# Optimization experiments

Hardware: AMD Instinct MI355X
Metric: run time of the kernel (lower is better)

Reference implementation:

```python
import jax, jax.numpy as jnp
import numpy as np

FREQ = 10000.0

def _abs_pos(T, d, freq):
    # AP[t, 2i] = sin(t / freq**(2i/d)), AP[t, 2i+1] = cos(...), i in [0, T//2)
    pos = jnp.arange(T, dtype=jnp.float32)[:, None]          # [T,1]
    i = jnp.arange(T // 2, dtype=jnp.float32)[None, :]       # [1,T/2]
    angle = pos / (freq ** (2.0 * i / d))                    # [T,T/2]
    return jnp.stack([jnp.sin(angle), jnp.cos(angle)], axis=-1).reshape(T, T)

def setup_inputs() -> dict:
    key = jax.random.key(0)
    k0, k1, k2, k3, k4 = jax.random.split(key, 5)
    T, d, H, dh = 4096, 1024, 8, 128
    s = 1.0 / np.sqrt(d).astype(np.float32)
    return {
        "x": jax.random.normal(k0, (T, d), jnp.float32),
        "Wq": jax.random.normal(k1, (H, dh, d), jnp.float32) * s,
        "Wk": jax.random.normal(k2, (H, dh, d), jnp.float32) * s,
        "Wv": jax.random.normal(k3, (H, dh, d), jnp.float32) * s,
        "Wout": jax.random.normal(k4, (d, H * dh), jnp.float32) * s,
    }

def reference(x, Wq, Wk, Wv, Wout):
    # x: [T,d]; Wq/Wk/Wv: [H,dh,d] (torch Linear weight layout, bias=False); Wout: [d, H*dh]
    T, d = x.shape
    Q = jnp.einsum('td,hed->hte', x, Wq)                     # [H,T,dh]
    K = jnp.einsum('td,hed->hte', x, Wk)
    V = jnp.einsum('td,hed->hte', x, Wv)
    energies = jnp.einsum('hte,hse->hts', Q, K)              # [H,T,T] (no 1/sqrt(dh) scaling, as in source)
    energies = energies + _abs_pos(T, d, FREQ)[None]         # absolute sinusoidal bias added to scores
    att = jax.nn.softmax(energies, axis=-1)                  # [H,T,T]
    # dropout(p=0.5) is identity in eval mode; reference runs in eval mode
    y = jnp.einsum('hts,hse->hte', att, V)                   # [H,T,dh]
    y = jnp.transpose(y, (1, 0, 2)).reshape(T, -1)           # concat heads along feature dim -> [T, H*dh]
    y = y @ Wout.T                                           # [T,d]
    return y, att[-1]                                        # source returns last head's att_weights
```

## Files before the change

### kernel.cpp

```cpp
#include <hip/hip_runtime.h>
#include <math.h>

#define Tn 4096
#define Dm 1024
#define Hn 8
#define DH 128

typedef __bf16 bf16x8 __attribute__((ext_vector_type(8)));
typedef float f32x4 __attribute__((ext_vector_type(4)));

#define LOG2E 1.4426950408889634f
#define WEXP 0.025952563241307518f
#define WDECAY 0.31622776601683794f
#define PIO2 1.5707963267948966f

#define MFMA(a, b, c) __builtin_amdgcn_mfma_f32_16x16x32_bf16((a), (b), (c), 0, 0, 0)

#define GLOAD_LDS(g, l) __builtin_amdgcn_global_load_lds( \
    (__attribute__((address_space(1))) void*)(void*)(g),  \
    (__attribute__((address_space(3))) void*)(l), 16, 0, 0)

__global__ __launch_bounds__(256)
void split_kernel(const float* __restrict__ in, __bf16* __restrict__ hi,
                  __bf16* __restrict__ lo, int n4) {
    int idx = blockIdx.x * 256 + threadIdx.x;
    if (idx >= n4) return;
    float4 v = ((const float4*)in)[idx];
    __attribute__((aligned(8))) __bf16 h[4], l[4];
    h[0] = (__bf16)v.x; h[1] = (__bf16)v.y; h[2] = (__bf16)v.z; h[3] = (__bf16)v.w;
    l[0] = (__bf16)(v.x - (float)h[0]);
    l[1] = (__bf16)(v.y - (float)h[1]);
    l[2] = (__bf16)(v.z - (float)h[2]);
    l[3] = (__bf16)(v.w - (float)h[3]);
    *(float2*)&hi[(size_t)idx * 4] = *(float2*)h;
    *(float2*)&lo[(size_t)idx * 4] = *(float2*)l;
}

__global__ __launch_bounds__(256)
void vtrans_kernel(const __bf16* __restrict__ V, __bf16* __restrict__ Vt) {
    __shared__ __bf16 tile[64][80];
    int h = blockIdx.z, t0 = blockIdx.x * 64, e0 = blockIdx.y * 64;
    const __bf16* Vh = V + (size_t)h * Tn * DH;
    __bf16* Vth = Vt + (size_t)h * DH * Tn;
#pragma unroll
    for (int p = 0; p < 2; ++p) {
        int r = (threadIdx.x >> 3) + p * 32;
        int c = (threadIdx.x & 7) * 8;
        *(float4*)&tile[r][c] = *(const float4*)&Vh[(size_t)(t0 + r) * DH + e0 + c];
    }
    __syncthreads();
#pragma unroll
    for (int p = 0; p < 2; ++p) {
        int r = (threadIdx.x >> 3) + p * 32;
        int c = (threadIdx.x & 7) * 8;
        __attribute__((aligned(16))) __bf16 tmp[8];
#pragma unroll
        for (int j = 0; j < 8; ++j) tmp[j] = tile[c + j][r];
        *(float4*)&Vth[(size_t)(e0 + r) * Tn + t0 + c] = *(float4*)tmp;
    }
}

__device__ __forceinline__
void gemm_body(__bf16 (*smem)[128 * 32],
               const __bf16* __restrict__ Ahi, const __bf16* __restrict__ Alo,
               const __bf16* __restrict__ Bhi, const __bf16* __restrict__ Blo,
               int ldA, int ldB, int K, int m0, int n0, f32x4 acc[4][4]) {
    int tid = threadIdx.x;
    int lane = tid & 63, wid = tid >> 6;
    int wm = (wid >> 1) * 64, wn = (wid & 1) * 64;
    int lm = lane & 15, q = lane >> 4;
    int lr = lane >> 2;
    int lc = (lane & 3) * 8;
    const bool split = (Alo != nullptr);
    for (int k0 = 0; k0 < K; k0 += 32) {
        __syncthreads();
#pragma unroll
        for (int p = 0; p < 128; p += 64) {
            int rb = p + wid * 16;
            int r = rb + lr;
            GLOAD_LDS(&Ahi[(size_t)(m0 + r) * ldA + k0 + lc], &smem[0][rb * 32]);
            GLOAD_LDS(&Bhi[(size_t)(n0 + r) * ldB + k0 + lc], &smem[2][rb * 32]);
            if (split) {
                GLOAD_LDS(&Alo[(size_t)(m0 + r) * ldA + k0 + lc], &smem[1][rb * 32]);
                GLOAD_LDS(&Blo[(size_t)(n0 + r) * ldB + k0 + lc], &smem[3][rb * 32]);
            }
        }
        __syncthreads();
        bf16x8 ah[4], bh[4], al[4], bl[4];
#pragma unroll
        for (int mt = 0; mt < 4; ++mt) {
            ah[mt] = *(const bf16x8*)&smem[0][(wm + mt * 16 + lm) * 32 + q * 8];
            if (split)
                al[mt] = *(const bf16x8*)&smem[1][(wm + mt * 16 + lm) * 32 + q * 8];
        }
#pragma unroll
        for (int nt = 0; nt < 4; ++nt) {
            bh[nt] = *(const bf16x8*)&smem[2][(wn + nt * 16 + lm) * 32 + q * 8];
            if (split)
                bl[nt] = *(const bf16x8*)&smem[3][(wn + nt * 16 + lm) * 32 + q * 8];
        }
#pragma unroll
        for (int mt = 0; mt < 4; ++mt)
#pragma unroll
            for (int nt = 0; nt < 4; ++nt) {
                acc[mt][nt] = MFMA(ah[mt], bh[nt], acc[mt][nt]);
                if (split) {
                    acc[mt][nt] = MFMA(ah[mt], bl[nt], acc[mt][nt]);
                    acc[mt][nt] = MFMA(al[mt], bh[nt], acc[mt][nt]);
                }
            }
    }
}

__global__ __launch_bounds__(256)
void qkv_kernel(const __bf16* __restrict__ xhi, const __bf16* __restrict__ xlo,
                const __bf16* __restrict__ Wqh, const __bf16* __restrict__ Wql,
                const __bf16* __restrict__ Wkh, const __bf16* __restrict__ Wkl,
                const __bf16* __restrict__ Wvh, const __bf16* __restrict__ Wvl,
                __bf16* __restrict__ Qh, __bf16* __restrict__ Ql,
                __bf16* __restrict__ Kh, __bf16* __restrict__ Kl,
                __bf16* __restrict__ Vb) {
    __shared__ __align__(16) __bf16 smem[4][128 * 32];
    int z = blockIdx.z;
    const __bf16* Bh = (z == 0) ? Wqh : (z == 1) ? Wkh : Wvh;
    const __bf16* Bl = (z == 0) ? Wql : (z == 1) ? Wkl : Wvl;
    __bf16* Oh = (z == 0) ? Qh : (z == 1) ? Kh : Vb;
    __bf16* Ol = (z == 0) ? Ql : (z == 1) ? Kl : nullptr;
    int m0 = blockIdx.y * 128, n0 = blockIdx.x * 128;
    int tid = threadIdx.x, lane = tid & 63, wid = tid >> 6;
    int wm = (wid >> 1) * 64, wn = (wid & 1) * 64;
    int lm = lane & 15, q = lane >> 4;
    f32x4 acc[4][4];
#pragma unroll
    for (int i = 0; i < 4; ++i)
#pragma unroll
        for (int j = 0; j < 4; ++j) acc[i][j] = (f32x4){0.f, 0.f, 0.f, 0.f};
    gemm_body(smem, xhi, xlo, Bh, Bl, Dm, Dm, Dm, m0, n0, acc);
#pragma unroll
    for (int mt = 0; mt < 4; ++mt)
#pragma unroll
        for (int r = 0; r < 4; ++r) {
            int grow = m0 + wm + mt * 16 + q * 4 + r;
#pragma unroll
            for (int nt = 0; nt < 4; ++nt) {
                int gc = n0 + wn + nt * 16 + lm;
                int h = gc >> 7, e = gc & 127;
                size_t o = ((size_t)h * Tn + grow) * DH + e;
                float v = acc[mt][nt][r];
                __bf16 hv = (__bf16)v;
                Oh[o] = hv;
                if (Ol) Ol[o] = (__bf16)(v - (float)hv);
            }
        }
}

__global__ __launch_bounds__(256)
void gemm_out(const __bf16* __restrict__ Ahi, const __bf16* __restrict__ Alo,
              const __bf16* __restrict__ Bhi, const __bf16* __restrict__ Blo,
              float* __restrict__ C) {
    __shared__ __align__(16) __bf16 smem[4][128 * 32];
    int m0 = blockIdx.y * 128, n0 = blockIdx.x * 128;
    int tid = threadIdx.x, lane = tid & 63, wid = tid >> 6;
    int wm = (wid >> 1) * 64, wn = (wid & 1) * 64;
    int lm = lane & 15, q = lane >> 4;
    f32x4 acc[4][4];
#pragma unroll
    for (int i = 0; i < 4; ++i)
#pragma unroll
        for (int j = 0; j < 4; ++j) acc[i][j] = (f32x4){0.f, 0.f, 0.f, 0.f};
    gemm_body(smem, Ahi, Alo, Bhi, Blo, Dm, Dm, Dm, m0, n0, acc);
#pragma unroll
    for (int mt = 0; mt < 4; ++mt)
#pragma unroll
        for (int r = 0; r < 4; ++r) {
            int grow = m0 + wm + mt * 16 + q * 4 + r;
#pragma unroll
            for (int nt = 0; nt < 4; ++nt)
                C[(size_t)grow * Dm + n0 + wn + nt * 16 + lm] = acc[mt][nt][r];
        }
}

__global__ __launch_bounds__(256, 2)
void flash_kernel(const __bf16* __restrict__ Qhi, const __bf16* __restrict__ Qlo,
                  const __bf16* __restrict__ Khi, const __bf16* __restrict__ Klo,
                  const __bf16* __restrict__ Vt, float* __restrict__ Opart,
                  float* __restrict__ mPart, float* __restrict__ lPart) {
    __shared__ __bf16 Ks[2][2][128][40];
    __shared__ __bf16 Ps[64][132];
    int bid = blockIdx.x;
    int h = bid & 7;
    int g = (bid >> 3) & 1;
    int m0 = (bid >> 4) * 64;
    int it0 = g * 16;
    const size_t TD = (size_t)Tn * DH;
    const __bf16* Qh = Qhi + h * TD;
    const __bf16* Ql = Qlo + h * TD;
    const __bf16* Kh = Khi + h * TD;
    const __bf16* Kl = Klo + h * TD;
    const __bf16* Vh = Vt + h * TD;
    float* Og = Opart + (size_t)g * Tn * Dm;

    int tid = threadIdx.x;
    int lane = tid & 63, wid = tid >> 6;
    int lm = lane & 15, q = lane >> 4;
    int wr0 = wid * 16;

    bf16x8 qfh[4], qfl[4];
#pragma unroll
    for (int kc = 0; kc < 4; ++kc) {
        size_t o = (size_t)(m0 + wr0 + lm) * DH + kc * 32 + q * 8;
        qfh[kc] = *(const bf16x8*)&Qh[o];
        qfl[kc] = *(const bf16x8*)&Ql[o];
    }

    f32x4 accO[8];
#pragma unroll
    for (int nt = 0; nt < 8; ++nt) accO[nt] = (f32x4){0.f, 0.f, 0.f, 0.f};
    float mrow[4], lrow[4];
#pragma unroll
    for (int r = 0; r < 4; ++r) { mrow[r] = -3.0e38f; lrow[r] = 0.f; }

    int sr = tid >> 2;
    int scc = (tid & 3) * 8;
    bool iscos = (lm & 1);
    float wv[8];
#pragma unroll
    for (int nt = 0; nt < 8; ++nt)
        wv[nt] = exp2f(-(float)(((g << 11) + nt * 16 + lm) >> 1) * WEXP);
    float tf[4];
#pragma unroll
    for (int r = 0; r < 4; ++r) tf[r] = (float)(m0 + wr0 + q * 4 + r);

    size_t voff[8];
#pragma unroll
    for (int nt = 0; nt < 8; ++nt)
        voff[nt] = (size_t)(nt * 16 + lm) * Tn + q * 8;

    float4 kh0, kl0, kh1, kl1;
    {
        size_t go0 = (size_t)(it0 * 128 + sr) * DH + scc;
        size_t go1 = go0 + (size_t)64 * DH;
        kh0 = *(const float4*)&Kh[go0];
        kl0 = *(const float4*)&Kl[go0];
        kh1 = *(const float4*)&Kh[go1];
        kl1 = *(const float4*)&Kl[go1];
    }

    for (int it = it0; it < it0 + 16; ++it) {
        int s0 = it * 128;
        f32x4 accS[8];
#pragma unroll
        for (int nt = 0; nt < 8; ++nt) accS[nt] = (f32x4){0.f, 0.f, 0.f, 0.f};

#pragma unroll
        for (int kc = 0; kc < 4; ++kc) {
            int b = kc & 1;
            *(float4*)&Ks[b][0][sr][scc]      = kh0;
            *(float4*)&Ks[b][1][sr][scc]      = kl0;
            *(float4*)&Ks[b][0][sr + 64][scc] = kh1;
            *(float4*)&Ks[b][1][sr + 64][scc] = kl1;
            __syncthreads();
            {
                int itn = (kc < 3) ? it : ((it < it0 + 15) ? it + 1 : it);
                int kcn = (kc < 3) ? kc + 1 : 0;
                size_t go0 = (size_t)(itn * 128 + sr) * DH + kcn * 32 + scc;
                size_t go1 = go0 + (size_t)64 * DH;
                kh0 = *(const float4*)&Kh[go0];
                kl0 = *(const float4*)&Kl[go0];
                kh1 = *(const float4*)&Kh[go1];
                kl1 = *(const float4*)&Kl[go1];
            }
            __builtin_amdgcn_s_setprio(1);
#pragma unroll
            for (int nt = 0; nt < 8; ++nt) {
                bf16x8 bh = *(const bf16x8*)&Ks[b][0][nt * 16 + lm][q * 8];
                bf16x8 bl = *(const bf16x8*)&Ks[b][1][nt * 16 + lm][q * 8];
                accS[nt] = MFMA(qfh[kc], bh, accS[nt]);
                accS[nt] = MFMA(qfh[kc], bl, accS[nt]);
                accS[nt] = MFMA(qfl[kc], bh, accS[nt]);
            }
            __builtin_amdgcn_s_setprio(0);
        }

        bf16x8 vrel[8];
#pragma unroll
        for (int nt = 0; nt < 8; ++nt)
            vrel[nt] = *(const bf16x8*)&Vh[voff[nt] + s0];

        float rmax[4];
#pragma unroll
        for (int r = 0; r < 4; ++r) {
            float mx = -3.0e38f;
#pragma unroll
            for (int nt = 0; nt < 8; ++nt) {
                float ang = tf[r] * wv[nt];
                float b = __sinf(iscos ? ang + PIO2 : ang);
                float v = accS[nt][r] + b;
                accS[nt][r] = v;
                mx = fmaxf(mx, v);
            }
            rmax[r] = mx;
        }
#pragma unroll
        for (int off = 1; off < 16; off <<= 1)
#pragma unroll
            for (int r = 0; r < 4; ++r)
                rmax[r] = fmaxf(rmax[r], __shfl_xor(rmax[r], off));
        float alpha[4], rsum[4];
#pragma unroll
        for (int r = 0; r < 4; ++r) {
            float mn = fmaxf(mrow[r], rmax[r]);
            alpha[r] = exp2f((mrow[r] - mn) * LOG2E);
            mrow[r] = mn;
            rsum[r] = 0.f;
        }
#pragma unroll
        for (int nt = 0; nt < 8; ++nt)
#pragma unroll
            for (int r = 0; r < 4; ++r) {
                float p = exp2f((accS[nt][r] - mrow[r]) * LOG2E);
                accS[nt][r] = p;
                rsum[r] += p;
            }
#pragma unroll
        for (int off = 1; off < 16; off <<= 1)
#pragma unroll
            for (int r = 0; r < 4; ++r)
                rsum[r] += __shfl_xor(rsum[r], off);
#pragma unroll
        for (int r = 0; r < 4; ++r)
            lrow[r] = lrow[r] * alpha[r] + rsum[r];
#pragma unroll
        for (int nt = 0; nt < 8; ++nt)
#pragma unroll
            for (int r = 0; r < 4; ++r)
                accO[nt][r] *= alpha[r];

#pragma unroll
        for (int nt = 0; nt < 8; ++nt)
#pragma unroll
            for (int r = 0; r < 4; ++r)
                Ps[wr0 + q * 4 + r][nt * 16 + lm] = (__bf16)accS[nt][r];

#pragma unroll
        for (int kc = 0; kc < 4; ++kc) {
            bf16x8 pa = *(const bf16x8*)&Ps[wr0 + lm][kc * 32 + q * 8];
            bf16x8 vcur[8];
#pragma unroll
            for (int nt = 0; nt < 8; ++nt) vcur[nt] = vrel[nt];
            if (kc < 3) {
#pragma unroll
                for (int nt = 0; nt < 8; ++nt)
                    vrel[nt] = *(const bf16x8*)&Vh[voff[nt] + s0 + (kc + 1) * 32];
            }
            __builtin_amdgcn_s_setprio(1);
#pragma unroll
            for (int nt = 0; nt < 8; ++nt)
                accO[nt] = MFMA(pa, vcur[nt], accO[nt]);
            __builtin_amdgcn_s_setprio(0);
        }

#pragma unroll
        for (int nt = 0; nt < 8; ++nt) wv[nt] *= WDECAY;
    }

#pragma unroll
    for (int r = 0; r < 4; ++r) {
        int t = m0 + wr0 + q * 4 + r;
#pragma unroll
        for (int nt = 0; nt < 8; ++nt)
            Og[(size_t)t * Dm + h * DH + nt * 16 + lm] = accO[nt][r];
        if (lm == 0) {
            mPart[(size_t)(g * Hn + h) * Tn + t] = mrow[r];
            lPart[(size_t)(g * Hn + h) * Tn + t] = lrow[r];
        }
    }
}

__global__ __launch_bounds__(256)
void combine_kernel(const float* __restrict__ Opart,
                    const float* __restrict__ mPart, const float* __restrict__ lPart,
                    __bf16* __restrict__ yhi, __bf16* __restrict__ ylo,
                    float* __restrict__ mM, float* __restrict__ lL) {
    int idx = blockIdx.x * 256 + threadIdx.x;
    int t = idx >> 8;
    int c4 = idx & 255;
    int c = c4 * 4;
    int h = c >> 7;
    float m0 = mPart[(size_t)h * Tn + t];
    float m1 = mPart[(size_t)(Hn + h) * Tn + t];
    float l0 = lPart[(size_t)h * Tn + t];
    float l1 = lPart[(size_t)(Hn + h) * Tn + t];
    float m = fmaxf(m0, m1);
    float w0 = exp2f((m0 - m) * LOG2E);
    float w1 = exp2f((m1 - m) * LOG2E);
    float l = l0 * w0 + l1 * w1;
    float inv = 1.0f / l;
    w0 *= inv; w1 *= inv;
    float4 a = ((const float4*)Opart)[idx];
    float4 b = ((const float4*)(Opart + (size_t)Tn * Dm))[idx];
    float y[4] = {a.x * w0 + b.x * w1, a.y * w0 + b.y * w1,
                  a.z * w0 + b.z * w1, a.w * w0 + b.w * w1};
    __attribute__((aligned(8))) __bf16 hh[4], ll[4];
#pragma unroll
    for (int j = 0; j < 4; ++j) {
        hh[j] = (__bf16)y[j];
        ll[j] = (__bf16)(y[j] - (float)hh[j]);
    }
    *(float2*)&yhi[(size_t)idx * 4] = *(float2*)hh;
    *(float2*)&ylo[(size_t)idx * 4] = *(float2*)ll;
    if (h == 7 && (c & 127) == 0) { mM[t] = m; lL[t] = l; }
}

__global__ __launch_bounds__(256)
void att_kernel(const __bf16* __restrict__ Ahi, const __bf16* __restrict__ Alo,
                const __bf16* __restrict__ Bhi, const __bf16* __restrict__ Blo,
                const float* __restrict__ mM, const float* __restrict__ lL,
                float* __restrict__ att) {
    __shared__ __align__(16) char shraw[34816];
    __bf16 (*smem)[128 * 32] = reinterpret_cast<__bf16(*)[128 * 32]>(shraw);
    float (*Ls)[68] = reinterpret_cast<float(*)[68]>(shraw);

    int m0 = blockIdx.y * 128, n0 = blockIdx.x * 128;
    int tid = threadIdx.x, lane = tid & 63, wid = tid >> 6;
    int wm = (wid >> 1) * 64, wn = (wid & 1) * 64;
    int lm = lane & 15, q = lane >> 4;
    f32x4 acc[4][4];
#pragma unroll
    for (int i = 0; i < 4; ++i)
#pragma unroll
        for (int j = 0; j < 4; ++j) acc[i][j] = (f32x4){0.f, 0.f, 0.f, 0.f};
    gemm_body(smem, Ahi, Alo, Bhi, Blo, DH, DH, DH, m0, n0, acc);

    float wv[4];
#pragma unroll
    for (int nt = 0; nt < 4; ++nt) {
        int s = n0 + wn + nt * 16 + lm;
        wv[nt] = exp2f(-(float)(s >> 1) * WEXP);
    }
    int par = lm & 1;
#pragma unroll
    for (int mt = 0; mt < 4; ++mt)
#pragma unroll
        for (int r = 0; r < 4; ++r) {
            int t = m0 + wm + mt * 16 + q * 4 + r;
            float tf = (float)t;
            float mr = mM[t];
            float linv = 1.0f / lL[t];
#pragma unroll
            for (int nt = 0; nt < 4; ++nt) {
                float ang = tf * wv[nt];
                float bias = __sinf(par ? ang + PIO2 : ang);
                acc[mt][nt][r] = exp2f((acc[mt][nt][r] + bias - mr) * LOG2E) * linv;
            }
        }

#pragma unroll
    for (int p = 0; p < 2; ++p) {
        __syncthreads();
        if ((wid & 1) == p) {
#pragma unroll
            for (int mt = 0; mt < 4; ++mt)
#pragma unroll
                for (int r = 0; r < 4; ++r)
#pragma unroll
                    for (int nt = 0; nt < 4; ++nt)
                        Ls[wm + mt * 16 + q * 4 + r][nt * 16 + lm] = acc[mt][nt][r];
        }
        __syncthreads();
#pragma unroll
        for (int j = 0; j < 8; ++j) {
            int row = j * 16 + (tid >> 4);
            int col = (tid & 15) * 4;
            float4 v = *(float4*)&Ls[row][col];
            *(float4*)&att[(size_t)(m0 + row) * Tn + n0 + p * 64 + col] = v;
        }
    }
}

extern "C" void kernel_launch(void* const* d_in, const int* in_sizes, int n_in,
                              void* d_out, int out_size, void* d_ws, size_t ws_size,
                              hipStream_t stream) {
    (void)in_sizes; (void)n_in; (void)out_size; (void)ws_size;
    const float* x    = (const float*)d_in[0];
    const float* Wq   = (const float*)d_in[1];
    const float* Wk   = (const float*)d_in[2];
    const float* Wv   = (const float*)d_in[3];
    const float* Wout = (const float*)d_in[4];

    float* out_y   = (float*)d_out;
    float* out_att = out_y + (size_t)Tn * Dm;

    const size_t MB = 1ull << 20;
    char* W = (char*)d_ws;
    __bf16* xhi  = (__bf16*)(W + 0 * MB);
    __bf16* xlo  = (__bf16*)(W + 8 * MB);
    __bf16* Wqhi = (__bf16*)(W + 16 * MB);
    __bf16* Wqlo = (__bf16*)(W + 18 * MB);
    __bf16* Wkhi = (__bf16*)(W + 20 * MB);
    __bf16* Wklo = (__bf16*)(W + 22 * MB);
    __bf16* Wvhi = (__bf16*)(W + 24 * MB);
    __bf16* Wvlo = (__bf16*)(W + 26 * MB);
    __bf16* Wohi = (__bf16*)(W + 28 * MB);
    __bf16* Wolo = (__bf16*)(W + 30 * MB);
    __bf16* Qhi  = (__bf16*)(W + 32 * MB);
    __bf16* Qlo  = (__bf16*)(W + 40 * MB);
    __bf16* Khi  = (__bf16*)(W + 48 * MB);
    __bf16* Klo  = (__bf16*)(W + 56 * MB);
    __bf16* Vb   = (__bf16*)(W + 64 * MB);
    __bf16* Vt   = (__bf16*)(W + 72 * MB);
    float*  mM    = (float*)(W + 80 * MB);
    float*  lL    = (float*)(W + 81 * MB);
    float*  mPart = (float*)(W + 82 * MB);
    float*  lPart = (float*)(W + 83 * MB);
    float*  Opart = (float*)(W + 84 * MB);
    __bf16* yhhi  = (__bf16*)(W + 116 * MB);
    __bf16* yhlo  = (__bf16*)(W + 124 * MB);

    dim3 blk(256);

    split_kernel<<<dim3(Tn * Dm / 4 / 256), blk, 0, stream>>>(x, xhi, xlo, Tn * Dm / 4);
    split_kernel<<<dim3(Dm * Dm / 4 / 256), blk, 0, stream>>>(Wq, Wqhi, Wqlo, Dm * Dm / 4);
    split_kernel<<<dim3(Dm * Dm / 4 / 256), blk, 0, stream>>>(Wk, Wkhi, Wklo, Dm * Dm / 4);
    split_kernel<<<dim3(Dm * Dm / 4 / 256), blk, 0, stream>>>(Wv, Wvhi, Wvlo, Dm * Dm / 4);
    split_kernel<<<dim3(Dm * Dm / 4 / 256), blk, 0, stream>>>(Wout, Wohi, Wolo, Dm * Dm / 4);

    qkv_kernel<<<dim3(Dm / 128, Tn / 128, 3), blk, 0, stream>>>(
        xhi, xlo, Wqhi, Wqlo, Wkhi, Wklo, Wvhi, Wvlo,
        Qhi, Qlo, Khi, Klo, Vb);
    vtrans_kernel<<<dim3(Tn / 64, DH / 64, Hn), blk, 0, stream>>>(Vb, Vt);

    flash_kernel<<<dim3(1024), blk, 0, stream>>>(Qhi, Qlo, Khi, Klo, Vt,
                                                 Opart, mPart, lPart);

    combine_kernel<<<dim3(Tn * Dm / 4 / 256), blk, 0, stream>>>(
        Opart, mPart, lPart, yhhi, yhlo, mM, lL);

    const size_t TD = (size_t)Tn * DH;
    att_kernel<<<dim3(Tn / 128, Tn / 128), blk, 0, stream>>>(
        Qhi + 7 * TD, Qlo + 7 * TD, Khi + 7 * TD, Klo + 7 * TD, mM, lL, out_att);

    gemm_out<<<dim3(Dm / 128, Tn / 128), blk, 0, stream>>>(yhhi, yhlo, Wohi, Wolo, out_y);
}
```

Measured before the change: 610.0 us.

## Stage QKV epilogue through LDS for coalesced stores; prefetch K two chunks ahead

The QKV projection epilogue now writes the bf16 hi and lo tiles into shared memory first, then stores whole 128-byte rows to global memory with vector writes, replacing scattered 2-byte stores. In the flash kernel, K chunks are register-prefetched two stages ahead using two alternating register sets instead of one, which gives each global load more time to arrive before its LDS write. This costs extra barriers in the epilogue and more registers in the flash kernel, which runs at two blocks per SM.

```diff
diff --git a/kernel.cpp b/kernel.cpp
--- a/kernel.cpp
+++ b/kernel.cpp
@@ -136,22 +136,48 @@
 #pragma unroll
         for (int j = 0; j < 4; ++j) acc[i][j] = (f32x4){0.f, 0.f, 0.f, 0.f};
     gemm_body(smem, xhi, xlo, Bh, Bl, Dm, Dm, Dm, m0, n0, acc);
+
+    __bf16* St = (__bf16*)smem;
+    int h0 = n0 >> 7;
+    int row = tid >> 1, half = (tid & 1) * 64;
+
+    __syncthreads();
 #pragma unroll
     for (int mt = 0; mt < 4; ++mt)
 #pragma unroll
-        for (int r = 0; r < 4; ++r) {
-            int grow = m0 + wm + mt * 16 + q * 4 + r;
-#pragma unroll
-            for (int nt = 0; nt < 4; ++nt) {
-                int gc = n0 + wn + nt * 16 + lm;
-                int h = gc >> 7, e = gc & 127;
-                size_t o = ((size_t)h * Tn + grow) * DH + e;
-                float v = acc[mt][nt][r];
-                __bf16 hv = (__bf16)v;
-                Oh[o] = hv;
-                if (Ol) Ol[o] = (__bf16)(v - (float)hv);
-            }
-        }
+        for (int r = 0; r < 4; ++r)
+#pragma unroll
+            for (int nt = 0; nt < 4; ++nt)
+                St[(wm + mt * 16 + q * 4 + r) * 128 + wn + nt * 16 + lm] =
+                    (__bf16)acc[mt][nt][r];
+    __syncthreads();
+    {
+        __bf16* dst = Oh + ((size_t)h0 * Tn + m0 + row) * DH + half;
+        const __bf16* src = St + row * 128 + half;
+#pragma unroll
+        for (int j = 0; j < 8; ++j)
+            *(float4*)&dst[j * 8] = *(const float4*)&src[j * 8];
+    }
+    if (Ol) {
+        __syncthreads();
+#pragma unroll
+        for (int mt = 0; mt < 4; ++mt)
+#pragma unroll
+            for (int r = 0; r < 4; ++r)
+#pragma unroll
+                for (int nt = 0; nt < 4; ++nt) {
+                    float v = acc[mt][nt][r];
+                    __bf16 hv = (__bf16)v;
+                    St[(wm + mt * 16 + q * 4 + r) * 128 + wn + nt * 16 + lm] =
+                        (__bf16)(v - (float)hv);
+                }
+        __syncthreads();
+        __bf16* dst = Ol + ((size_t)h0 * Tn + m0 + row) * DH + half;
+        const __bf16* src = St + row * 128 + half;
+#pragma unroll
+        for (int j = 0; j < 8; ++j)
+            *(float4*)&dst[j * 8] = *(const float4*)&src[j * 8];
+    }
 }
 
 __global__ __launch_bounds__(256)
@@ -179,6 +205,33 @@
                 C[(size_t)grow * Dm + n0 + wn + nt * 16 + lm] = acc[mt][nt][r];
         }
 }
+
+#define QK_STEP(SET, BUF, QIDX, NIT, NKC)                                     \
+    {                                                                          \
+        *(float4*)&Ks[BUF][0][sr][scc]      = SET##h0;                         \
+        *(float4*)&Ks[BUF][1][sr][scc]      = SET##l0;                         \
+        *(float4*)&Ks[BUF][0][sr + 64][scc] = SET##h1;                         \
+        *(float4*)&Ks[BUF][1][sr + 64][scc] = SET##l1;                         \
+        __syncthreads();                                                       \
+        {                                                                      \
+            size_t go0 = (size_t)((NIT) * 128 + sr) * DH + (NKC) * 32 + scc;   \
+            size_t go1 = go0 + (size_t)64 * DH;                                \
+            SET##h0 = *(const float4*)&Kh[go0];                                \
+            SET##l0 = *(const float4*)&Kl[go0];                                \
+            SET##h1 = *(const float4*)&Kh[go1];                                \
+            SET##l1 = *(const float4*)&Kl[go1];                                \
+        }                                                                      \
+        __builtin_amdgcn_s_setprio(1);                                         \
+        _Pragma("unroll")                                                      \
+        for (int nt = 0; nt < 8; ++nt) {                                       \
+            bf16x8 kbh = *(const bf16x8*)&Ks[BUF][0][nt * 16 + lm][q * 8];     \
+            bf16x8 kbl = *(const bf16x8*)&Ks[BUF][1][nt * 16 + lm][q * 8];     \
+            accS[nt] = MFMA(qfh[QIDX], kbh, accS[nt]);                         \
+            accS[nt] = MFMA(qfh[QIDX], kbl, accS[nt]);                         \
+            accS[nt] = MFMA(qfl[QIDX], kbh, accS[nt]);                         \
+        }                                                                      \
+        __builtin_amdgcn_s_setprio(0);                                         \
+    }
 
 __global__ __launch_bounds__(256, 2)
 void flash_kernel(const __bf16* __restrict__ Qhi, const __bf16* __restrict__ Qlo,
@@ -236,51 +289,28 @@
     for (int nt = 0; nt < 8; ++nt)
         voff[nt] = (size_t)(nt * 16 + lm) * Tn + q * 8;
 
-    float4 kh0, kl0, kh1, kl1;
+    float4 kah0, kal0, kah1, kal1, kbh0, kbl0, kbh1, kbl1;
     {
-        size_t go0 = (size_t)(it0 * 128 + sr) * DH + scc;
-        size_t go1 = go0 + (size_t)64 * DH;
-        kh0 = *(const float4*)&Kh[go0];
-        kl0 = *(const float4*)&Kl[go0];
-        kh1 = *(const float4*)&Kh[go1];
-        kl1 = *(const float4*)&Kl[go1];
+        size_t g0 = (size_t)(it0 * 128 + sr) * DH + scc;
+        size_t g1 = g0 + (size_t)64 * DH;
+        kah0 = *(const float4*)&Kh[g0]; kal0 = *(const float4*)&Kl[g0];
+        kah1 = *(const float4*)&Kh[g1]; kal1 = *(const float4*)&Kl[g1];
+        size_t h0_ = g0 + 32, h1_ = g1 + 32;
+        kbh0 = *(const float4*)&Kh[h0_]; kbl0 = *(const float4*)&Kl[h0_];
+        kbh1 = *(const float4*)&Kh[h1_]; kbl1 = *(const float4*)&Kl[h1_];
     }
 
     for (int it = it0; it < it0 + 16; ++it) {
         int s0 = it * 128;
+        int itn = (it < it0 + 15) ? it + 1 : it;
         f32x4 accS[8];
 #pragma unroll
         for (int nt = 0; nt < 8; ++nt) accS[nt] = (f32x4){0.f, 0.f, 0.f, 0.f};
 
-#pragma unroll
-        for (int kc = 0; kc < 4; ++kc) {
-            int b = kc & 1;
-            *(float4*)&Ks[b][0][sr][scc]      = kh0;
-            *(float4*)&Ks[b][1][sr][scc]      = kl0;
-            *(float4*)&Ks[b][0][sr + 64][scc] = kh1;
-            *(float4*)&Ks[b][1][sr + 64][scc] = kl1;
-            __syncthreads();
-            {
-                int itn = (kc < 3) ? it : ((it < it0 + 15) ? it + 1 : it);
-                int kcn = (kc < 3) ? kc + 1 : 0;
-                size_t go0 = (size_t)(itn * 128 + sr) * DH + kcn * 32 + scc;
-                size_t go1 = go0 + (size_t)64 * DH;
-                kh0 = *(const float4*)&Kh[go0];
-                kl0 = *(const float4*)&Kl[go0];
-                kh1 = *(const float4*)&Kh[go1];
-                kl1 = *(const float4*)&Kl[go1];
-            }
-            __builtin_amdgcn_s_setprio(1);
-#pragma unroll
-            for (int nt = 0; nt < 8; ++nt) {
-                bf16x8 bh = *(const bf16x8*)&Ks[b][0][nt * 16 + lm][q * 8];
-                bf16x8 bl = *(const bf16x8*)&Ks[b][1][nt * 16 + lm][q * 8];
-                accS[nt] = MFMA(qfh[kc], bh, accS[nt]);
-                accS[nt] = MFMA(qfh[kc], bl, accS[nt]);
-                accS[nt] = MFMA(qfl[kc], bh, accS[nt]);
-            }
-            __builtin_amdgcn_s_setprio(0);
-        }
+        QK_STEP(ka, 0, 0, it, 2)
+        QK_STEP(kb, 1, 1, it, 3)
+        QK_STEP(ka, 0, 2, itn, 0)
+        QK_STEP(kb, 1, 3, itn, 1)
 
         bf16x8 vrel[8];
 #pragma unroll
```

Result: no change. 610.9 us (+0.1%).
